# Kernel tuning notes

Measured on AMD Instinct MI355X. Metric: run time of the kernel, lower is better.

## Reference

```python
import jax, jax.numpy as jnp
import numpy as np


def setup_inputs() -> dict:
    key = jax.random.key(0)
    ks = jax.random.split(key, 7)
    B, T, D, H = 32, 512, 512, 512
    return {
        "x": jax.random.normal(ks[0], (B, T, D), dtype=jnp.float32),
        "W_Du": jax.random.normal(ks[1], (D, H), dtype=jnp.float32) * (1.0 / np.sqrt(D)),
        "W_Dr1": jax.random.normal(ks[2], (D, H), dtype=jnp.float32) * (1.0 / np.sqrt(D)),
        "W_Dr2": jax.random.normal(ks[3], (D, H), dtype=jnp.float32) * (1.0 / np.sqrt(D)),
        "b_Du": jax.random.normal(ks[4], (H,), dtype=jnp.float32) * 0.02,
        "b_Dr1": jax.random.normal(ks[5], (H,), dtype=jnp.float32) * 0.02,
        "b_Dr2": jax.random.normal(ks[6], (H,), dtype=jnp.float32) * 0.02,
    }


def reference(x, W_Du, W_Dr1, W_Dr2, b_Du, b_Dr1, b_Dr2):
    # Precompute all per-step projections across time (batched matmuls),
    # then run the strictly sequential gated recurrence with lax.scan.
    r1 = jax.nn.softmax(jnp.einsum('btd,dh->bth', x, W_Dr1) + b_Dr1, axis=-1)  # [B,T,H]
    r2 = jax.nn.softmax(jnp.einsum('btd,dh->bth', x, W_Dr2) + b_Dr2, axis=-1)  # [B,T,H]
    u = jnp.tanh(jnp.einsum('btd,dh->bth', x, W_Du) + b_Du)                     # [B,T,H]

    def step(s, inp):
        r1t, r2t, ut = inp
        s_new = r1t * s + r2t * ut
        return s_new, s_new

    init = jnp.zeros((x.shape[0], W_Du.shape[1]), dtype=x.dtype)
    # time-major for scan: [T,B,H]
    _, ys = jax.lax.scan(
        step, init,
        (jnp.swapaxes(r1, 0, 1), jnp.swapaxes(r2, 0, 1), jnp.swapaxes(u, 0, 1)),
    )
    return jnp.swapaxes(ys, 0, 1)  # [B,T,H]
```

## Files before the change

kernel.cpp:

```cpp
#include <hip/hip_runtime.h>
#include <hip/hip_bf16.h>

#define B_N 32
#define T_N 512
#define D_N 512
#define H_N 512
#define M_N (B_N * T_N)

typedef __attribute__((ext_vector_type(8))) short bf16x8;
typedef __attribute__((ext_vector_type(4))) float f32x4;

__device__ __forceinline__ unsigned short f2bf(float f) {
  unsigned u = __float_as_uint(f);
  u += 0x7FFFu + ((u >> 16) & 1u);
  return (unsigned short)(u >> 16);
}
__device__ __forceinline__ unsigned short f2h(float f) {
  _Float16 h = (_Float16)f;
  return *(unsigned short*)&h;
}
__device__ __forceinline__ float h2f(unsigned short u) {
  _Float16 h = *(_Float16*)&u;
  return (float)h;
}

#define GLOAD16(g, l) __builtin_amdgcn_global_load_lds( \
    (const __attribute__((address_space(1))) void*)(g), \
    (__attribute__((address_space(3))) void*)(l), 16, 0, 0)

__global__ void prep_kernel(const float* __restrict__ x,
                            const float* __restrict__ W0,
                            const float* __restrict__ W1,
                            const float* __restrict__ W2,
                            unsigned short* __restrict__ xb,
                            unsigned short* __restrict__ Wt,
                            float* __restrict__ S) {
  int blk = blockIdx.x;
  int tid = threadIdx.x;
  if (blk < 768) {
    __shared__ float tile[32][33];
    int id = blk >> 8;
    int t = blk & 255;
    int kr = (t >> 4) << 5;
    int nc = (t & 15) << 5;
    const float* W = (id == 0) ? W0 : (id == 1) ? W1 : W2;
    unsigned short* Wo = Wt + (size_t)id * (D_N * H_N);
    int tx = tid & 31, ty0 = tid >> 5;
    for (int ty = ty0; ty < 32; ty += 8)
      tile[ty][tx] = W[(size_t)(kr + ty) * H_N + nc + tx];
    __syncthreads();
    for (int ty = ty0; ty < 32; ty += 8)
      Wo[(size_t)(nc + ty) * D_N + kr + tx] = f2bf(tile[tx][ty]);
  } else if (blk < 2816) {
    int b = blk - 768;
    const float4* xv = (const float4*)x;
#pragma unroll
    for (int u = 0; u < 4; ++u) {
      int i = b * 1024 + u * 256 + tid;
      float4 v = xv[i];
      ushort4 o;
      o.x = f2bf(v.x); o.y = f2bf(v.y); o.z = f2bf(v.z); o.w = f2bf(v.w);
      ((ushort4*)xb)[i] = o;
    }
  } else {
    ((float4*)S)[(blk - 2816) * 256 + tid] = (float4){0.f, 0.f, 0.f, 0.f};
  }
}

__global__ __launch_bounds__(256) void gemm3(
    const unsigned short* __restrict__ xb,
    const unsigned short* __restrict__ Wt,
    const float* __restrict__ bDu,
    const float* __restrict__ bDr1,
    const float* __restrict__ bDr2,
    unsigned short* __restrict__ uP,
    unsigned short* __restrict__ e1P,
    unsigned short* __restrict__ e2P,
    float* __restrict__ S1,
    float* __restrict__ S2) {
  __shared__ __align__(16) char smem[65536];

  const int tid = threadIdx.x;
  const int lane = tid & 63;
  const int wv = tid >> 6;
  const int wr = wv >> 1;
  const int wc = wv & 1;
  const int g = lane >> 4;
  const int c16 = lane & 15;

  const int m0 = blockIdx.x * 128;
  const int n0 = blockIdx.y * 128;
  const int id = blockIdx.z;
  const unsigned short* Wp = Wt + (size_t)id * (D_N * H_N);

  f32x4 acc[4][4];
#pragma unroll
  for (int mt = 0; mt < 4; ++mt)
#pragma unroll
    for (int nt = 0; nt < 4; ++nt)
      acc[mt][nt] = (f32x4){0.f, 0.f, 0.f, 0.f};

  const int rowoff = tid >> 3;
  const int lsl = ((tid & 7) ^ ((tid >> 3) & 7)) * 8;
  const unsigned short* aSrc = xb + (size_t)(m0 + rowoff) * D_N + lsl;
  const unsigned short* bSrc = Wp + (size_t)(n0 + rowoff) * D_N + lsl;
  const int dstOff = wv * 1024;

  const int h3 = c16 & 7;

#define STAGE(buf, kstep) do {                                           \
    const int k0_ = (kstep) * 64;                                        \
    _Pragma("unroll")                                                    \
    for (int i = 0; i < 4; ++i)                                          \
      GLOAD16(aSrc + (size_t)i * (32 * D_N) + k0_,                       \
              smem + (buf) * 16384 + dstOff + i * 4096);                 \
    _Pragma("unroll")                                                    \
    for (int i = 0; i < 4; ++i)                                          \
      GLOAD16(bSrc + (size_t)i * (32 * D_N) + k0_,                       \
              smem + 32768 + (buf) * 16384 + dstOff + i * 4096);         \
  } while (0)

#define COMPUTE(buf) do {                                                \
    _Pragma("unroll")                                                    \
    for (int kh = 0; kh < 2; ++kh) {                                     \
      const int soff = ((kh * 4 + g) ^ h3) << 4;                         \
      bf16x8 af[4], bb[4];                                               \
      _Pragma("unroll")                                                  \
      for (int mt = 0; mt < 4; ++mt)                                     \
        af[mt] = *(const bf16x8*)(smem + (buf) * 16384 +                 \
                                  (wr * 64 + mt * 16 + c16) * 128 + soff); \
      _Pragma("unroll")                                                  \
      for (int nt = 0; nt < 4; ++nt)                                     \
        bb[nt] = *(const bf16x8*)(smem + 32768 + (buf) * 16384 +         \
                                  (wc * 64 + nt * 16 + c16) * 128 + soff); \
      _Pragma("unroll")                                                  \
      for (int mt = 0; mt < 4; ++mt)                                     \
        _Pragma("unroll")                                                \
        for (int nt = 0; nt < 4; ++nt)                                   \
          acc[mt][nt] = __builtin_amdgcn_mfma_f32_16x16x32_bf16(         \
              af[mt], bb[nt], acc[mt][nt], 0, 0, 0);                     \
    }                                                                    \
  } while (0)

#define WB(n) do {                                                       \
    __builtin_amdgcn_sched_barrier(0);                                   \
    asm volatile("s_waitcnt vmcnt(" #n ")\n\ts_barrier" ::: "memory");   \
    __builtin_amdgcn_sched_barrier(0);                                   \
  } while (0)

#define SB do {                                                          \
    __builtin_amdgcn_sched_barrier(0);                                   \
    asm volatile("s_barrier" ::: "memory");                              \
    __builtin_amdgcn_sched_barrier(0);                                   \
  } while (0)

  STAGE(0, 0);
  STAGE(1, 1);
#pragma unroll 1
  for (int t = 0; t < 6; ++t) {
    WB(8);
    COMPUTE(t & 1);
    SB;
    STAGE(t & 1, t + 2);
  }
  WB(8);  COMPUTE(0);
  WB(0);  COMPUTE(1);

  const float* bp = (id == 0) ? bDu : (id == 1) ? bDr1 : bDr2;
  unsigned short* outp = (id == 0) ? uP : (id == 1) ? e1P : e2P;
  float* Sp = (id == 1) ? S1 : S2;
  float bias[4];
#pragma unroll
  for (int nt = 0; nt < 4; ++nt)
    bias[nt] = bp[n0 + wc * 64 + nt * 16 + c16];

#pragma unroll
  for (int mt = 0; mt < 4; ++mt)
#pragma unroll
    for (int i = 0; i < 4; ++i) {
      int row = m0 + wr * 64 + mt * 16 + g * 4 + i;
      unsigned short* op = outp + (size_t)row * H_N + n0 + wc * 64 + c16;
      if (id == 0) {
#pragma unroll
        for (int nt = 0; nt < 4; ++nt) {
          float z = acc[mt][nt][i] + bias[nt];
          float e = __expf(2.f * z);
          op[nt * 16] = f2h(1.f - 2.f * __builtin_amdgcn_rcpf(e + 1.f));
        }
      } else {
        float ps = 0.f;
#pragma unroll
        for (int nt = 0; nt < 4; ++nt) {
          float e = __expf(acc[mt][nt][i] + bias[nt]);
          op[nt * 16] = f2h(e);
          ps += e;
        }
        ps += __shfl_xor(ps, 1);
        ps += __shfl_xor(ps, 2);
        ps += __shfl_xor(ps, 4);
        ps += __shfl_xor(ps, 8);
        if (c16 == 0) atomicAdd(&Sp[row], ps);
      }
    }
#undef STAGE
#undef COMPUTE
#undef WB
#undef SB
}

__global__ void scan_pass1(const unsigned short* __restrict__ e1P,
                           const unsigned short* __restrict__ e2P,
                           const unsigned short* __restrict__ uP,
                           const float* __restrict__ S1,
                           const float* __restrict__ S2,
                           float* __restrict__ cP,
                           float* __restrict__ cS) {
  __shared__ float ls1[64], ls2[64];
  int gt = blockIdx.x * 256 + threadIdx.x;
  int chunk = gt >> 14;
  int r = gt & 16383;
  int b = r >> 9, h = r & 511;
  int row0 = b * T_N + chunk * 64;
  if (threadIdx.x < 64) ls1[threadIdx.x] = 1.f / S1[row0 + threadIdx.x];
  else if (threadIdx.x < 128) ls2[threadIdx.x - 64] = 1.f / S2[row0 + threadIdx.x - 64];
  __syncthreads();
  size_t idx = (size_t)row0 * H_N + h;
  float p = 1.f, s = 0.f;
#pragma unroll 4
  for (int j = 0; j < 64; ++j) {
    float a = ls1[j] * h2f(e1P[idx]);
    float cu = ls2[j] * h2f(e2P[idx]) * h2f(uP[idx]);
    s = fmaf(a, s, cu);
    p *= a;
    idx += H_N;
  }
  cP[gt] = p;
  cS[gt] = s;
}

__global__ void scan_pass3(const unsigned short* __restrict__ e1P,
                           const unsigned short* __restrict__ e2P,
                           const unsigned short* __restrict__ uP,
                           const float* __restrict__ S1,
                           const float* __restrict__ S2,
                           const float* __restrict__ cP,
                           const float* __restrict__ cS,
                           float* __restrict__ out) {
  __shared__ float ls1[64], ls2[64];
  int gt = blockIdx.x * 256 + threadIdx.x;
  int chunk = gt >> 14;
  int r = gt & 16383;
  int b = r >> 9, h = r & 511;
  int row0 = b * T_N + chunk * 64;
  if (threadIdx.x < 64) ls1[threadIdx.x] = 1.f / S1[row0 + threadIdx.x];
  else if (threadIdx.x < 128) ls2[threadIdx.x - 64] = 1.f / S2[row0 + threadIdx.x - 64];
  float s = 0.f;
  for (int c2 = 0; c2 < chunk; ++c2)
    s = fmaf(cP[c2 * 16384 + r], s, cS[c2 * 16384 + r]);
  __syncthreads();
  size_t idx = (size_t)row0 * H_N + h;
#pragma unroll 4
  for (int j = 0; j < 64; ++j) {
    float a = ls1[j] * h2f(e1P[idx]);
    float cu = ls2[j] * h2f(e2P[idx]) * h2f(uP[idx]);
    s = fmaf(a, s, cu);
    out[idx] = s;
    idx += H_N;
  }
}

extern "C" void kernel_launch(void* const* d_in, const int* in_sizes, int n_in,
                              void* d_out, int out_size, void* d_ws, size_t ws_size,
                              hipStream_t stream) {
  const float* x  = (const float*)d_in[0];
  const float* W0 = (const float*)d_in[1];
  const float* W1 = (const float*)d_in[2];
  const float* W2 = (const float*)d_in[3];
  const float* b0 = (const float*)d_in[4];
  const float* b1 = (const float*)d_in[5];
  const float* b2 = (const float*)d_in[6];
  float* out = (float*)d_out;

  char* ws = (char*)d_ws;
  unsigned short* xb  = (unsigned short*)ws;
  unsigned short* Wt  = (unsigned short*)(ws + 16777216);
  unsigned short* uP  = (unsigned short*)(ws + 18350080);
  unsigned short* e1P = (unsigned short*)(ws + 35127296);
  unsigned short* e2P = (unsigned short*)(ws + 51904512);
  float*          S1  = (float*)(ws + 68681728);
  float*          S2  = (float*)(ws + 68747264);
  float*          cP  = (float*)(ws + 68812800);
  float*          cS  = (float*)(ws + 69337088);

  prep_kernel<<<2848, 256, 0, stream>>>(x, W0, W1, W2, xb, Wt, S1);
  gemm3<<<dim3(128, 4, 3), 256, 0, stream>>>(xb, Wt, b0, b1, b2,
                                             uP, e1P, e2P, S1, S2);
  scan_pass1<<<512, 256, 0, stream>>>(e1P, e2P, uP, S1, S2, cP, cS);
  scan_pass3<<<512, 256, 0, stream>>>(e1P, e2P, uP, S1, S2, cP, cS, out);
}
```

Before: 79.87 us.

## Remap GEMM grid for XCD-aware tile locality and simplify double-buffer pipeline

The 3D grid becomes a 1D grid of 1536 blocks. Block indices are remapped so that consecutive blocks placed on the same XCD (blockIdx & 7) cover neighbouring M tiles across all three weights and all N tiles, which should improve L2 reuse of the x rows. The hand-written vmcnt/s_barrier pipeline, which prefetched two stages ahead, is replaced by a plain one-ahead double buffer using __syncthreads. This makes the loop simpler but may expose more global-load latency, because only one stage is in flight and every barrier waits on all outstanding loads.

```diff
diff --git a/kernel.cpp b/kernel.cpp
--- a/kernel.cpp
+++ b/kernel.cpp
@@ -80,6 +80,12 @@
     float* __restrict__ S2) {
   __shared__ __align__(16) char smem[65536];
 
+  const int wg = (blockIdx.x & 7) * 192 + (blockIdx.x >> 3);
+  const int bx = wg / 12;
+  const int rzy = wg - bx * 12;
+  const int id = rzy >> 2;
+  const int by = rzy & 3;
+
   const int tid = threadIdx.x;
   const int lane = tid & 63;
   const int wv = tid >> 6;
@@ -88,9 +94,8 @@
   const int g = lane >> 4;
   const int c16 = lane & 15;
 
-  const int m0 = blockIdx.x * 128;
-  const int n0 = blockIdx.y * 128;
-  const int id = blockIdx.z;
+  const int m0 = bx * 128;
+  const int n0 = by * 128;
   const unsigned short* Wp = Wt + (size_t)id * (D_N * H_N);
 
   f32x4 acc[4][4];
@@ -142,29 +147,15 @@
     }                                                                    \
   } while (0)
 
-#define WB(n) do {                                                       \
-    __builtin_amdgcn_sched_barrier(0);                                   \
-    asm volatile("s_waitcnt vmcnt(" #n ")\n\ts_barrier" ::: "memory");   \
-    __builtin_amdgcn_sched_barrier(0);                                   \
-  } while (0)
-
-#define SB do {                                                          \
-    __builtin_amdgcn_sched_barrier(0);                                   \
-    asm volatile("s_barrier" ::: "memory");                              \
-    __builtin_amdgcn_sched_barrier(0);                                   \
-  } while (0)
-
   STAGE(0, 0);
-  STAGE(1, 1);
+  __syncthreads();
 #pragma unroll 1
-  for (int t = 0; t < 6; ++t) {
-    WB(8);
-    COMPUTE(t & 1);
-    SB;
-    STAGE(t & 1, t + 2);
-  }
-  WB(8);  COMPUTE(0);
-  WB(0);  COMPUTE(1);
+  for (int t = 0; t < 8; ++t) {
+    const int buf = t & 1;
+    if (t < 7) STAGE(buf ^ 1, t + 1);
+    COMPUTE(buf);
+    __syncthreads();
+  }
 
   const float* bp = (id == 0) ? bDu : (id == 1) ? bDr1 : bDr2;
   unsigned short* outp = (id == 0) ? uP : (id == 1) ? e1P : e2P;
@@ -204,8 +195,6 @@
     }
 #undef STAGE
 #undef COMPUTE
-#undef WB
-#undef SB
 }
 
 __global__ void scan_pass1(const unsigned short* __restrict__ e1P,
@@ -293,8 +282,7 @@
   float*          cS  = (float*)(ws + 69337088);
 
   prep_kernel<<<2848, 256, 0, stream>>>(x, W0, W1, W2, xb, Wt, S1);
-  gemm3<<<dim3(128, 4, 3), 256, 0, stream>>>(xb, Wt, b0, b1, b2,
-                                             uP, e1P, e2P, S1, S2);
+  gemm3<<<1536, 256, 0, stream>>>(xb, Wt, b0, b1, b2, uP, e1P, e2P, S1, S2);
   scan_pass1<<<512, 256, 0, stream>>>(e1P, e2P, uP, S1, S2, cP, cS);
   scan_pass3<<<512, 256, 0, stream>>>(e1P, e2P, uP, S1, S2, cP, cS, out);
 }
```

Result: slower. 82.22 us (+2.9%).
